# Optimization experiments

Hardware: AMD Instinct MI355X
Metric: run time of the kernel (lower is better)

Reference implementation:

```python
import jax, jax.numpy as jnp
import numpy as np
from jax import lax

N_NODES = 116
N_EDGES = 1160
D_FEAT = 653  # SAGEConv in/out channels (last dim)


def _sage_max(x, src, dst, w_l, w_r, b):
    # PyG SAGEConv(aggr='max'): out = lin_l(max_j x_j) + lin_r(x)
    # x: [N, C, F]; aggregation over incoming edges per target node.
    msgs = x[src]  # [E, C, F]
    agg = jax.ops.segment_max(msgs, dst, num_segments=N_NODES)
    agg = jnp.where(jnp.isfinite(agg), agg, 0.0)  # empty segments -> 0 (PyG behavior)
    return jnp.einsum('ncf,gf->ncg', agg, w_l) + b + jnp.einsum('ncf,gf->ncg', x, w_r)


def setup_inputs() -> dict:
    key = jax.random.key(0)
    ks = jax.random.split(key, 16)
    inp = {}
    inp['x'] = jax.random.normal(ks[0], (N_NODES, 64, 657), dtype=jnp.float32)
    inp['edge_index'] = jax.random.randint(ks[1], (2, N_EDGES), 0, N_NODES, dtype=jnp.int64)
    # Conv1d(64 -> 256, kernel=5, groups=4): weight [256, 16, 5]
    inp['conv_w'] = jax.random.normal(ks[2], (256, 16, 5), dtype=jnp.float32) * 0.05
    inp['conv_b'] = jax.random.normal(ks[3], (256,), dtype=jnp.float32) * 0.05
    s = 1.0 / np.sqrt(D_FEAT)
    inp['sage_wl'] = jax.random.normal(ks[4], (D_FEAT, D_FEAT), dtype=jnp.float32) * s
    inp['sage_wr'] = jax.random.normal(ks[5], (D_FEAT, D_FEAT), dtype=jnp.float32) * s
    inp['sage_b'] = jnp.zeros((D_FEAT,), dtype=jnp.float32)
    inp['fc1_w'] = jax.random.normal(ks[6], (128, D_FEAT), dtype=jnp.float32) * s
    inp['fc1_b'] = jnp.zeros((128,), dtype=jnp.float32)
    inp['fc2_w'] = jax.random.normal(ks[7], (32, 128), dtype=jnp.float32) * (1.0 / np.sqrt(128))
    inp['fc2_b'] = jnp.zeros((32,), dtype=jnp.float32)
    inp['fc3_w'] = jax.random.normal(ks[8], (4, 32), dtype=jnp.float32) * (1.0 / np.sqrt(32))
    inp['fc3_b'] = jnp.zeros((4,), dtype=jnp.float32)
    return inp


def reference(x, edge_index, conv_w, conv_b, sage_wl, sage_wr, sage_b,
              fc1_w, fc1_b, fc2_w, fc2_b, fc3_w, fc3_b):
    # grouped Conv1d: [N,64,657] -> [N,256,653]
    h = lax.conv_general_dilated(
        x, conv_w, window_strides=(1,), padding='VALID',
        dimension_numbers=('NCH', 'OIH', 'NCH'), feature_group_count=4)
    h = h + conv_b[None, :, None]
    src, dst = edge_index[0], edge_index[1]
    for _ in range(3):  # same SAGEConv layer applied three times
        h = _sage_max(h, src, dst, sage_wl, sage_wr, sage_b)
    # global_mean_pool over the single graph (batch all zeros) then squeeze
    h = h.mean(axis=0)  # [256, 653]
    h = jax.nn.gelu(h @ fc1_w.T + fc1_b, approximate=False)
    h = jax.nn.gelu(h @ fc2_w.T + fc2_b, approximate=False)
    h = h @ fc3_w.T + fc3_b  # [256, 4]
    return jax.nn.softmax(h, axis=1)
```

## Files before the change

kernel.cpp:

```cpp
#include <hip/hip_runtime.h>
#include <hip/hip_bf16.h>
#include <math.h>

#define NN 116
#define NE 1160
#define CCH 256
#define FF 653
#define KP 672
#define MM (NN*CCH)
#define NPAD 768
#define SZH ((size_t)MM*KP)

typedef unsigned short ushort;
typedef short bf16x8 __attribute__((ext_vector_type(8)));
typedef float f32x4 __attribute__((ext_vector_type(4)));

__device__ __forceinline__ float bfbits_to_f(ushort u) {
    unsigned int w = ((unsigned int)u) << 16;
    return __uint_as_float(w);
}
__device__ __forceinline__ ushort f_to_bfbits(float f) {
    unsigned int u = __float_as_uint(f);
    u += 0x7FFFu + ((u >> 16) & 1u);
    return (ushort)(u >> 16);
}

__device__ __forceinline__ void gl_lds16(const void* g, void* l) {
    __builtin_amdgcn_global_load_lds(
        (const __attribute__((address_space(1))) unsigned int*)g,
        (__attribute__((address_space(3))) unsigned int*)l, 16, 0, 0);
}

__global__ void build_csr_k(const int* __restrict__ ei, int* __restrict__ off,
                            int* __restrict__ lst) {
    __shared__ int s_cnt[NN];
    __shared__ int s_off[NN + 1];
    int t = threadIdx.x;
    for (int i = t; i < NN; i += blockDim.x) s_cnt[i] = 0;
    __syncthreads();
    for (int e = t; e < NE; e += blockDim.x) atomicAdd(&s_cnt[ei[NE + e]], 1);
    __syncthreads();
    if (t == 0) {
        s_off[0] = 0;
        for (int i = 0; i < NN; ++i) s_off[i + 1] = s_off[i] + s_cnt[i];
    }
    __syncthreads();
    for (int i = t; i < NN; i += blockDim.x) { off[i] = s_off[i]; s_cnt[i] = 0; }
    if (t == 0) off[NN] = s_off[NN];
    __syncthreads();
    for (int e = t; e < NE; e += blockDim.x) {
        int d = ei[NE + e];
        int p = atomicAdd(&s_cnt[d], 1);
        lst[s_off[d] + p] = ei[e];
    }
}

__global__ void build_wc_k(const float* __restrict__ wl, const float* __restrict__ wr,
                           ushort* __restrict__ wc) {
    int idx = blockIdx.x * 256 + threadIdx.x;
    const int total = 2 * NPAD * KP;
    if (idx >= total) return;
    int k = idx % KP;
    int rem = idx / KP;
    int n = rem % NPAD;
    int p = rem / NPAD;
    float v = 0.f;
    if (n < FF && k < FF) v = (p ? wr : wl)[(size_t)n * FF + k];
    wc[idx] = f_to_bfbits(v);
}

__global__ __launch_bounds__(256) void conv1d_k(
    const float* __restrict__ x, const float* __restrict__ w,
    const float* __restrict__ b, ushort* __restrict__ h) {
    const int f  = blockIdx.x * 256 + threadIdx.x;
    if (f >= KP) return;
    const int n  = blockIdx.y;
    const int oc = blockIdx.z;
    const int o0 = oc * 16;
    const int g  = o0 >> 6;
    if (f >= FF) {
#pragma unroll
        for (int oo = 0; oo < 16; ++oo)
            h[(size_t)(n * CCH + o0 + oo) * KP + f] = 0;
        return;
    }
    float xv[16][5];
    const float* xp = x + ((size_t)n * 64 + g * 16) * 657 + f;
#pragma unroll
    for (int i = 0; i < 16; ++i)
#pragma unroll
        for (int k = 0; k < 5; ++k)
            xv[i][k] = xp[i * 657 + k];
#pragma unroll
    for (int oo = 0; oo < 16; ++oo) {
        const int o = o0 + oo;
        const float* wp = w + o * 80;
        float acc = b[o];
#pragma unroll
        for (int i = 0; i < 16; ++i)
#pragma unroll
            for (int k = 0; k < 5; ++k)
                acc = fmaf(xv[i][k], wp[i * 5 + k], acc);
        h[(size_t)(n * CCH + o) * KP + f] = f_to_bfbits(acc);
    }
}

__global__ void seg_max_k(const ushort* __restrict__ h, ushort* __restrict__ agg,
                          const int* __restrict__ off, const int* __restrict__ lst) {
    int j = blockIdx.x * 256 + threadIdx.x;
    int c = j / 84;
    int chunk = j % 84;
    int n = blockIdx.y;
    int o0 = off[n], o1 = off[n + 1];
    size_t dsti = ((size_t)(n * CCH + c)) * KP + chunk * 8;
    if (o0 == o1) {
        *(uint4*)(agg + dsti) = make_uint4(0, 0, 0, 0);
        return;
    }
    float m[8];
#pragma unroll
    for (int i = 0; i < 8; ++i) m[i] = -3.4e38f;
    for (int e = o0; e < o1; ++e) {
        int s = lst[e];
        const uint4 v = *(const uint4*)(h + ((size_t)(s * CCH + c)) * KP + chunk * 8);
        unsigned int u[4] = {v.x, v.y, v.z, v.w};
#pragma unroll
        for (int q = 0; q < 4; ++q) {
            float lo = __uint_as_float(u[q] << 16);
            float hi = __uint_as_float(u[q] & 0xFFFF0000u);
            m[2*q]   = fmaxf(m[2*q],   lo);
            m[2*q+1] = fmaxf(m[2*q+1], hi);
        }
    }
    unsigned int o[4];
#pragma unroll
    for (int q = 0; q < 4; ++q) {
        unsigned int a = __float_as_uint(m[2*q])   >> 16;
        unsigned int bq = __float_as_uint(m[2*q+1]) & 0xFFFF0000u;
        o[q] = a | bq;
    }
    *(uint4*)(agg + dsti) = make_uint4(o[0], o[1], o[2], o[3]);
}

__global__ __launch_bounds__(256) void sage_gemm_k(
    const ushort* __restrict__ Agg, const ushort* __restrict__ Hcur,
    const ushort* __restrict__ Wc, const float* __restrict__ bias,
    ushort* __restrict__ Hnxt)
{
    __shared__ ushort As[128 * 32];
    __shared__ ushort Bs[128 * 32];
    const int tid  = threadIdx.x;
    const int lane = tid & 63;
    const int wid  = tid >> 6;
    const int bm = blockIdx.x * 128;
    const int bn = blockIdx.y * 128;
    const int wm = (wid >> 1) * 64;
    const int wn = (wid & 1) * 64;

    f32x4 acc[4][4];
#pragma unroll
    for (int i = 0; i < 4; ++i)
#pragma unroll
        for (int j = 0; j < 4; ++j) acc[i][j] = 0.f;

    const int srow = lane >> 2;
    const int schk = (lane & 3) * 8;
    ushort* lA = As + wid * 16 * 32;
    ushort* lB = Bs + wid * 16 * 32;
    const int lr = lane & 15;
    const int kc = (lane >> 4) * 8;

    for (int pass = 0; pass < 2; ++pass) {
        const ushort* Ab = pass ? Hcur : Agg;
        const ushort* Wb = Wc + (size_t)pass * NPAD * KP;
        for (int k0 = 0; k0 < KP; k0 += 32) {
            const ushort* ga0 = Ab + (size_t)(bm + wid * 16 + srow) * KP + k0 + schk;
            const ushort* gb0 = Wb + (size_t)(bn + wid * 16 + srow) * KP + k0 + schk;
            gl_lds16(ga0, lA);
            gl_lds16(ga0 + (size_t)64 * KP, lA + 64 * 32);
            gl_lds16(gb0, lB);
            gl_lds16(gb0 + (size_t)64 * KP, lB + 64 * 32);
            __syncthreads();
            bf16x8 af[4], bfr[4];
#pragma unroll
            for (int i = 0; i < 4; ++i)
                af[i] = *(const bf16x8*)&As[(wm + i * 16 + lr) * 32 + kc];
#pragma unroll
            for (int j = 0; j < 4; ++j)
                bfr[j] = *(const bf16x8*)&Bs[(wn + j * 16 + lr) * 32 + kc];
#pragma unroll
            for (int i = 0; i < 4; ++i)
#pragma unroll
                for (int j = 0; j < 4; ++j)
                    acc[i][j] = __builtin_amdgcn_mfma_f32_16x16x32_bf16(
                        af[i], bfr[j], acc[i][j], 0, 0, 0);
            __syncthreads();
        }
    }
    const int lg = lane >> 4;
#pragma unroll
    for (int j = 0; j < 4; ++j) {
        int n = bn + wn + j * 16 + lr;
        if (n >= KP) continue;
        bool valid = n < FF;
        float bv = valid ? bias[n] : 0.f;
#pragma unroll
        for (int i = 0; i < 4; ++i) {
#pragma unroll
            for (int r = 0; r < 4; ++r) {
                int m = bm + wm + i * 16 + lg * 4 + r;
                float v = valid ? (acc[i][j][r] + bv) : 0.f;
                Hnxt[(size_t)m * KP + n] = f_to_bfbits(v);
            }
        }
    }
}

__global__ void pool_k(const ushort* __restrict__ h, float* __restrict__ pool) {
    int j = blockIdx.x * 256 + threadIdx.x;
    if (j >= 256 * 84) return;
    int c = j / 84;
    int chunk = j % 84;
    float s[8];
#pragma unroll
    for (int i = 0; i < 8; ++i) s[i] = 0.f;
    for (int n = 0; n < NN; ++n) {
        const uint4 v = *(const uint4*)(h + ((size_t)(n * CCH + c)) * KP + chunk * 8);
        unsigned int u[4] = {v.x, v.y, v.z, v.w};
#pragma unroll
        for (int q = 0; q < 4; ++q) {
            s[2*q]   += __uint_as_float(u[q] << 16);
            s[2*q+1] += __uint_as_float(u[q] & 0xFFFF0000u);
        }
    }
    const float inv = 1.0f / NN;
    float* dst = pool + (size_t)c * KP + chunk * 8;
#pragma unroll
    for (int i = 0; i < 8; ++i) dst[i] = s[i] * inv;
}

__device__ __forceinline__ float gelu_exact(float v) {
    return 0.5f * v * (1.0f + erff(v * 0.70710678118654752f));
}

__global__ void head_k(const float* __restrict__ pool,
                       const float* __restrict__ w1, const float* __restrict__ b1,
                       const float* __restrict__ w2, const float* __restrict__ b2,
                       const float* __restrict__ w3, const float* __restrict__ b3,
                       float* __restrict__ out) {
    __shared__ float row[FF];
    __shared__ float h1[128];
    __shared__ float h2[32];
    __shared__ float sc[4];
    const int c = blockIdx.x;
    const int t = threadIdx.x;
    for (int i = t; i < FF; i += 128) row[i] = pool[(size_t)c * KP + i];
    __syncthreads();
    {
        const float* wp = w1 + (size_t)t * FF;
        float s = b1[t];
        for (int i = 0; i < FF; ++i) s = fmaf(row[i], wp[i], s);
        h1[t] = gelu_exact(s);
    }
    __syncthreads();
    if (t < 32) {
        const float* wp = w2 + (size_t)t * 128;
        float s = b2[t];
#pragma unroll
        for (int i = 0; i < 128; ++i) s = fmaf(h1[i], wp[i], s);
        h2[t] = gelu_exact(s);
    }
    __syncthreads();
    if (t < 4) {
        const float* wp = w3 + (size_t)t * 32;
        float s = b3[t];
#pragma unroll
        for (int i = 0; i < 32; ++i) s = fmaf(h2[i], wp[i], s);
        sc[t] = s;
    }
    __syncthreads();
    if (t < 4) {
        float mx = fmaxf(fmaxf(sc[0], sc[1]), fmaxf(sc[2], sc[3]));
        float e0 = __expf(sc[0] - mx), e1 = __expf(sc[1] - mx);
        float e2 = __expf(sc[2] - mx), e3 = __expf(sc[3] - mx);
        float inv = 1.0f / (e0 + e1 + e2 + e3);
        float ev = (t == 0) ? e0 : (t == 1) ? e1 : (t == 2) ? e2 : e3;
        out[(size_t)c * 4 + t] = ev * inv;
    }
}

extern "C" void kernel_launch(void* const* d_in, const int* in_sizes, int n_in,
                              void* d_out, int out_size, void* d_ws, size_t ws_size,
                              hipStream_t stream) {
    const float* x      = (const float*)d_in[0];
    const int*   ei     = (const int*)  d_in[1];
    const float* conv_w = (const float*)d_in[2];
    const float* conv_b = (const float*)d_in[3];
    const float* wl     = (const float*)d_in[4];
    const float* wr     = (const float*)d_in[5];
    const float* sb     = (const float*)d_in[6];
    const float* fc1w   = (const float*)d_in[7];
    const float* fc1b   = (const float*)d_in[8];
    const float* fc2w   = (const float*)d_in[9];
    const float* fc2b   = (const float*)d_in[10];
    const float* fc3w   = (const float*)d_in[11];
    const float* fc3b   = (const float*)d_in[12];
    float* out = (float*)d_out;

    ushort* hA  = (ushort*)d_ws;
    ushort* hB  = hA + SZH;
    ushort* agg = hB + SZH;
    ushort* wc  = agg + SZH;
    float*  pool = (float*)(wc + (size_t)2 * NPAD * KP);
    int*    off  = (int*)(pool + (size_t)CCH * KP);
    int*    lst  = off + 128;

    build_csr_k<<<1, 256, 0, stream>>>(ei, off, lst);
    build_wc_k<<<(2 * NPAD * KP + 255) / 256, 256, 0, stream>>>(wl, wr, wc);
    {
        dim3 cgrid((KP + 255) / 256, NN, 16);
        conv1d_k<<<cgrid, 256, 0, stream>>>(x, conv_w, conv_b, hA);
    }

    dim3 sg_grid(84, NN);
    dim3 gm_grid(MM / 128, NPAD / 128);
    ushort* cur = hA;
    ushort* nxt = hB;
    for (int layer = 0; layer < 3; ++layer) {
        seg_max_k<<<sg_grid, 256, 0, stream>>>(cur, agg, off, lst);
        sage_gemm_k<<<gm_grid, 256, 0, stream>>>(agg, cur, wc, sb, nxt);
        ushort* tmp = cur; cur = nxt; nxt = tmp;
    }
    pool_k<<<84, 256, 0, stream>>>(cur, pool);
    head_k<<<CCH, 128, 0, stream>>>(pool, fc1w, fc1b, fc2w, fc2b, fc3w, fc3b, out);
}
```

Measured before the change: 695.3 us.

## Stage conv input in shared memory and swizzle GEMM LDS chunk layout

The grouped Conv1d kernel now loads each node/group's 16 input channels into shared memory once. Each thread then computes 16 output channels over strided feature positions, so global x reloads are replaced by LDS reads, and the grid shrinks to 116x4 blocks of 512 threads. Separately, the SAGE GEMM XOR-swizzles the 8-element chunk index in its LDS tiles, on both the global-to-LDS store side and the fragment-read side, to reduce bank conflicts. The conv rewrite lowers launch parallelism and puts weight reads in the inner loop. The swizzle only stays correct if the gl_lds16 destination mapping matches the swizzled addresses.

```diff
diff --git a/kernel.cpp b/kernel.cpp
--- a/kernel.cpp
+++ b/kernel.cpp
@@ -69,39 +69,47 @@
     wc[idx] = f_to_bfbits(v);
 }
 
-__global__ __launch_bounds__(256) void conv1d_k(
+__global__ __launch_bounds__(512) void conv1d_k(
     const float* __restrict__ x, const float* __restrict__ w,
     const float* __restrict__ b, ushort* __restrict__ h) {
-    const int f  = blockIdx.x * 256 + threadIdx.x;
-    if (f >= KP) return;
-    const int n  = blockIdx.y;
-    const int oc = blockIdx.z;
-    const int o0 = oc * 16;
-    const int g  = o0 >> 6;
-    if (f >= FF) {
+    __shared__ float sx[16 * 657 + 32];
+    const int n = blockIdx.x;
+    const int g = blockIdx.y;
+    const int tid = threadIdx.x;
+    const float* xg = x + ((size_t)n * 64 + g * 16) * 657;
+    for (int i = tid; i < 16 * 657; i += 512) sx[i] = xg[i];
+    if (tid < 32) sx[16 * 657 + tid] = 0.f;
+    __syncthreads();
+    const int qc = tid >> 7;
+    const int fl = tid & 127;
+    const int o0 = g * 64 + qc * 16;
+    float bv[16];
+#pragma unroll
+    for (int oo = 0; oo < 16; ++oo) bv[oo] = b[o0 + oo];
+    const float* wq = w + o0 * 80;
+    for (int f = fl; f < KP; f += 128) {
+        float acc[16];
+#pragma unroll
+        for (int oo = 0; oo < 16; ++oo) acc[oo] = bv[oo];
+#pragma unroll
+        for (int i = 0; i < 16; ++i) {
+            float xv[5];
+#pragma unroll
+            for (int k = 0; k < 5; ++k) xv[k] = sx[i * 657 + f + k];
+#pragma unroll
+            for (int oo = 0; oo < 16; ++oo) {
+                const float* wp = wq + oo * 80 + i * 5;
+                acc[oo] = fmaf(xv[0], wp[0], acc[oo]);
+                acc[oo] = fmaf(xv[1], wp[1], acc[oo]);
+                acc[oo] = fmaf(xv[2], wp[2], acc[oo]);
+                acc[oo] = fmaf(xv[3], wp[3], acc[oo]);
+                acc[oo] = fmaf(xv[4], wp[4], acc[oo]);
+            }
+        }
+        const bool valid = f < FF;
 #pragma unroll
         for (int oo = 0; oo < 16; ++oo)
-            h[(size_t)(n * CCH + o0 + oo) * KP + f] = 0;
-        return;
-    }
-    float xv[16][5];
-    const float* xp = x + ((size_t)n * 64 + g * 16) * 657 + f;
-#pragma unroll
-    for (int i = 0; i < 16; ++i)
-#pragma unroll
-        for (int k = 0; k < 5; ++k)
-            xv[i][k] = xp[i * 657 + k];
-#pragma unroll
-    for (int oo = 0; oo < 16; ++oo) {
-        const int o = o0 + oo;
-        const float* wp = w + o * 80;
-        float acc = b[o];
-#pragma unroll
-        for (int i = 0; i < 16; ++i)
-#pragma unroll
-            for (int k = 0; k < 5; ++k)
-                acc = fmaf(xv[i][k], wp[i * 5 + k], acc);
-        h[(size_t)(n * CCH + o) * KP + f] = f_to_bfbits(acc);
+            h[(size_t)(n * CCH + o0 + oo) * KP + f] = valid ? f_to_bfbits(acc[oo]) : (ushort)0;
     }
 }
 
@@ -163,12 +171,14 @@
 #pragma unroll
         for (int j = 0; j < 4; ++j) acc[i][j] = 0.f;
 
-    const int srow = lane >> 2;
-    const int schk = (lane & 3) * 8;
+    const int srow   = lane >> 2;
+    const int schunk = lane & 3;
+    const int schk   = (schunk ^ ((srow >> 1) & 3)) * 8;
     ushort* lA = As + wid * 16 * 32;
     ushort* lB = Bs + wid * 16 * 32;
-    const int lr = lane & 15;
-    const int kc = (lane >> 4) * 8;
+    const int lr  = lane & 15;
+    const int cc  = lane >> 4;
+    const int kc  = (cc ^ ((lr >> 1) & 3)) * 8;
 
     for (int pass = 0; pass < 2; ++pass) {
         const ushort* Ab = pass ? Hcur : Agg;
@@ -318,8 +328,8 @@
     build_csr_k<<<1, 256, 0, stream>>>(ei, off, lst);
     build_wc_k<<<(2 * NPAD * KP + 255) / 256, 256, 0, stream>>>(wl, wr, wc);
     {
-        dim3 cgrid((KP + 255) / 256, NN, 16);
-        conv1d_k<<<cgrid, 256, 0, stream>>>(x, conv_w, conv_b, hA);
+        dim3 cgrid(NN, 4);
+        conv1d_k<<<cgrid, 512, 0, stream>>>(x, conv_w, conv_b, hA);
     }
 
     dim3 sg_grid(84, NN);
```

New measurement: 2.596 ms. 3.73x slower.
